# Optimization experiments

Measured on AMD Instinct MI355X. Metric: run time of the kernel, lower is better.

Reference implementation:

```python
import jax, jax.numpy as jnp
import numpy as np
from jax import lax

EPS = 1e-10
NUM_ITERATIONS = 3  # init arg num_iterations
M, R = 16384, 32


def setup_inputs() -> dict:
    key = jax.random.key(0)
    x = jax.random.normal(key, (M, R, 2), dtype=jnp.float32)
    return {"x": x}


def reference(x):
    # x: (M, R, 2) -> complex (M, R); work with QT (R, M) so rows = columns
    r = x.shape[1]
    xc = (x[..., 0] + 1j * x[..., 1]).T  # (R, M) complex64
    idx = jnp.arange(r)

    # --- classical Gram-Schmidt pass (sequential over columns j) ---
    def gs_col(QT, j):
        def proj(v, i):
            qi = QT[i]
            coeff = jnp.sum(jnp.conj(qi) * v) * (i < j)  # only previous cols
            return v - coeff * qi, None
        v, _ = lax.scan(proj, xc[j], idx)
        v = v / jnp.sqrt(jnp.sum(jnp.abs(v) ** 2) + EPS)
        return QT.at[j].set(v), None

    QT, _ = lax.scan(gs_col, jnp.zeros_like(xc), idx)

    # --- iterative refinement sweeps: each column uses the OLD Q -> vmap over j ---
    def refine_col(QT, j):
        def proj(v, i):
            qi = QT[i]
            coeff = jnp.sum(jnp.conj(qi) * v) * (i != j)
            return v - 0.5 * coeff * qi, None
        v, _ = lax.scan(proj, QT[j], idx)
        return v / jnp.sqrt(jnp.sum(jnp.abs(v) ** 2) + EPS)

    for _ in range(NUM_ITERATIONS):
        QT = jax.vmap(refine_col, in_axes=(None, 0))(QT, idx)

    Q = QT.T  # (M, R)
    return jnp.stack([Q.real, Q.imag], axis=-1)
```

## Files before the change

### kernel.cpp

```cpp
#include <hip/hip_runtime.h>


__device__ __forceinline__ float rdlane(float v, int lane) {
  return __builtin_bit_cast(
      float, __builtin_amdgcn_readlane(__builtin_bit_cast(int, v), lane));
}

__global__ __launch_bounds__(256) void gram_partial(const float* __restrict__ x,
                                                    float* __restrict__ G8) {
  __shared__ float lds[64 * 64];
  const int t = threadIdx.x;
  const int j = t & 31, g = t >> 5;
  const size_t row0 = (size_t)blockIdx.x * 64;
  float ar[4] = {0.f, 0.f, 0.f, 0.f};
  float ai[4] = {0.f, 0.f, 0.f, 0.f};
  const float4* src = (const float4*)(x + row0 * 64);
  float4* dst = (float4*)lds;
#pragma unroll
  for (int q = 0; q < 4; ++q) dst[t + 256 * q] = src[t + 256 * q];
  __syncthreads();
#pragma unroll 4
  for (int m = 0; m < 64; ++m) {
    const float2* row = (const float2*)(lds + m * 64);
    const float2 xj = row[j];
#pragma unroll
    for (int q = 0; q < 4; ++q) {
      const float2 xi = row[g + q * 8];
      ar[q] += xi.x * xj.x + xi.y * xj.y;
      ai[q] += xi.x * xj.y - xi.y * xj.x;
    }
  }
  float* P = G8 + (size_t)(blockIdx.x & 7) * 2048;
#pragma unroll
  for (int q = 0; q < 4; ++q) {
    const int i = g + q * 8;
    atomicAdd(&P[(i * 32 + j) * 2 + 0], ar[q]);
    atomicAdd(&P[(i * 32 + j) * 2 + 1], ai[q]);
  }
}

__global__ __launch_bounds__(64, 1) void solve32(const float* __restrict__ x,
                                                 const float* __restrict__ G8,
                                                 float* __restrict__ out) {
  __shared__ float4 xsp[32 * 17];
  __shared__ float2 Acm[33 * 32];
  const int t = threadIdx.x;
  const int j = t & 31;
  const size_t rowbase = (size_t)blockIdx.x * 32;

  const float4* src = (const float4*)(x + rowbase * 64);
#pragma unroll
  for (int s = 0; s < 8; ++s) {
    const int gi = t + 64 * s;
    xsp[(gi >> 4) * 17 + (gi & 15)] = src[gi];
  }

  {
    const float2* Gf2 = (const float2*)G8;
    float2 a[32];
#pragma unroll
    for (int i = 0; i < 32; ++i) {
      float2 s = Gf2[i * 32 + j];
#pragma unroll
      for (int c = 1; c < 8; ++c) {
        const float2 p = Gf2[c * 1024 + i * 32 + j];
        s.x += p.x;
        s.y += p.y;
      }
      a[i] = s;
    }
#pragma unroll
    for (int k = 0; k < 31; ++k) {
      const float invd = 1.0f / rdlane(a[k].x, k);
      const bool act = (j > k);
      const float ux = act ? a[k].x * invd : 0.0f;
      const float uy = act ? a[k].y * invd : 0.0f;
#pragma unroll
      for (int i = k + 1; i < 32; ++i) {
        const float cr = rdlane(a[i].x, k);
        const float ci = rdlane(a[i].y, k);
        a[i].x -= cr * ux - ci * uy;
        a[i].y -= cr * uy + ci * ux;
      }
    }
    if (t < 32) {
#pragma unroll
      for (int i = 0; i < 32; ++i) Acm[t * 33 + i] = a[i];
    }
  }
  __syncthreads();

  float2 xr[32];
#pragma unroll
  for (int q = 0; q < 16; ++q) {
    const float4 v = xsp[j * 17 + q];
    xr[2 * q].x = v.x; xr[2 * q].y = v.y;
    xr[2 * q + 1].x = v.z; xr[2 * q + 1].y = v.w;
  }
#pragma unroll
  for (int jj = 0; jj < 32; ++jj) {
    const float d = Acm[jj * 33 + jj].x;
    const float invd = 1.0f / d;
    const float invs = 1.0f / sqrtf(d);
    const float ux = xr[jj].x * invd, uy = xr[jj].y * invd;
    xr[jj].x *= invs;
    xr[jj].y *= invs;
#pragma unroll
    for (int i = jj + 1; i < 32; ++i) {
      const float2 l = Acm[jj * 33 + i];
      xr[i].x -= ux * l.x + uy * l.y;
      xr[i].y -= uy * l.x - ux * l.y;
    }
  }

  if (t < 32) {
#pragma unroll
    for (int q = 0; q < 16; ++q) {
      float4 v;
      v.x = xr[2 * q].x; v.y = xr[2 * q].y;
      v.z = xr[2 * q + 1].x; v.w = xr[2 * q + 1].y;
      xsp[t * 17 + q] = v;
    }
  }
  __syncthreads();
  float4* op = (float4*)(out + rowbase * 64);
#pragma unroll
  for (int s = 0; s < 8; ++s) {
    const int gi = t + 64 * s;
    op[gi] = xsp[(gi >> 4) * 17 + (gi & 15)];
  }
}

extern "C" void kernel_launch(void* const* d_in, const int* in_sizes, int n_in,
                              void* d_out, int out_size, void* d_ws, size_t ws_size,
                              hipStream_t stream) {
  const float* x = (const float*)d_in[0];
  float* out = (float*)d_out;
  float* G8 = (float*)d_ws;

  gram_partial<<<256, 256, 0, stream>>>(x, G8);
  solve32<<<512, 64, 0, stream>>>(x, G8, out);
}
```

Measured before the change: 94.62 us.

## Compute inverse Cholesky factor once and apply as a small GEMM

Instead of having each of the 512 blocks reduce the partial Gram matrices, factor them, and forward-substitute its own rows, a single block now builds the Cholesky factor and the 32x32 matrix that maps x to Q, writing it to workspace. A separate wide kernel then multiplies each row of x by this matrix. This removes the redundant per-block factorization and the serial triangular solve from the bulk pass. In exchange it adds a third launch and a serial single-block stage between the Gram and apply kernels.

After: 107.2 us. 13.2% more time.

```diff
diff --git a/kernel.cpp b/kernel.cpp
--- a/kernel.cpp
+++ b/kernel.cpp
@@ -39,21 +39,11 @@
   }
 }
 
-__global__ __launch_bounds__(64, 1) void solve32(const float* __restrict__ x,
-                                                 const float* __restrict__ G8,
-                                                 float* __restrict__ out) {
-  __shared__ float4 xsp[32 * 17];
+__global__ __launch_bounds__(128, 1) void chol_winv(const float* __restrict__ G8,
+                                                    float* __restrict__ Wg) {
   __shared__ float2 Acm[33 * 32];
   const int t = threadIdx.x;
   const int j = t & 31;
-  const size_t rowbase = (size_t)blockIdx.x * 32;
-
-  const float4* src = (const float4*)(x + rowbase * 64);
-#pragma unroll
-  for (int s = 0; s < 8; ++s) {
-    const int gi = t + 64 * s;
-    xsp[(gi >> 4) * 17 + (gi & 15)] = src[gi];
-  }
 
   {
     const float2* Gf2 = (const float2*)G8;
@@ -85,17 +75,17 @@
     }
     if (t < 32) {
 #pragma unroll
-      for (int i = 0; i < 32; ++i) Acm[t * 33 + i] = a[i];
+      for (int i = 0; i < 32; ++i) Acm[j * 33 + i] = a[i];
     }
   }
   __syncthreads();
 
+  const int c = j;
   float2 xr[32];
 #pragma unroll
-  for (int q = 0; q < 16; ++q) {
-    const float4 v = xsp[j * 17 + q];
-    xr[2 * q].x = v.x; xr[2 * q].y = v.y;
-    xr[2 * q + 1].x = v.z; xr[2 * q + 1].y = v.w;
+  for (int i = 0; i < 32; ++i) {
+    xr[i].x = (i == c) ? 1.0f : 0.0f;
+    xr[i].y = 0.0f;
   }
 #pragma unroll
   for (int jj = 0; jj < 32; ++jj) {
@@ -112,23 +102,39 @@
       xr[i].y -= uy * l.x - ux * l.y;
     }
   }
+  if (t < 32) {
+    float2* Wr = (float2*)Wg + c * 32;
+#pragma unroll
+    for (int i = 0; i < 32; ++i) Wr[i] = xr[i];
+  }
+}
 
-  if (t < 32) {
+__global__ __launch_bounds__(256) void apply_qr(const float* __restrict__ x,
+                                                const float* __restrict__ W,
+                                                float* __restrict__ out) {
+  __shared__ float w[2048];
+  __shared__ float xs[1024];
+  const int t = threadIdx.x;
+  ((float4*)w)[t] = ((const float4*)W)[t];
+  ((float4*)w)[t + 256] = ((const float4*)W)[t + 256];
+  const size_t m0 = (size_t)blockIdx.x * 16;
+  ((float4*)xs)[t] = ((const float4*)(x + m0 * 64))[t];
+  __syncthreads();
+  const int mloc = t >> 4, jp = t & 15;
+  const float2* xrow = (const float2*)(xs + mloc * 64);
+  float2 a0 = {0.f, 0.f}, a1 = {0.f, 0.f};
 #pragma unroll
-    for (int q = 0; q < 16; ++q) {
-      float4 v;
-      v.x = xr[2 * q].x; v.y = xr[2 * q].y;
-      v.z = xr[2 * q + 1].x; v.w = xr[2 * q + 1].y;
-      xsp[t * 17 + q] = v;
-    }
+  for (int i = 0; i < 32; ++i) {
+    const float2 xi = xrow[i];
+    const float4 wv = ((const float4*)(w + i * 64))[jp];
+    a0.x += xi.x * wv.x - xi.y * wv.y;
+    a0.y += xi.x * wv.y + xi.y * wv.x;
+    a1.x += xi.x * wv.z - xi.y * wv.w;
+    a1.y += xi.x * wv.w + xi.y * wv.z;
   }
-  __syncthreads();
-  float4* op = (float4*)(out + rowbase * 64);
-#pragma unroll
-  for (int s = 0; s < 8; ++s) {
-    const int gi = t + 64 * s;
-    op[gi] = xsp[(gi >> 4) * 17 + (gi & 15)];
-  }
+  float4 o;
+  o.x = a0.x; o.y = a0.y; o.z = a1.x; o.w = a1.y;
+  ((float4*)out)[(size_t)blockIdx.x * 256 + t] = o;
 }
 
 extern "C" void kernel_launch(void* const* d_in, const int* in_sizes, int n_in,
@@ -137,7 +143,9 @@
   const float* x = (const float*)d_in[0];
   float* out = (float*)d_out;
   float* G8 = (float*)d_ws;
+  float* Wg = (float*)d_ws + 16384;
 
   gram_partial<<<256, 256, 0, stream>>>(x, G8);
-  solve32<<<512, 64, 0, stream>>>(x, G8, out);
+  chol_winv<<<1, 128, 0, stream>>>(G8, Wg);
+  apply_qr<<<1024, 256, 0, stream>>>(x, Wg, out);
 }
```
